# Kernel tuning notes

Hardware: AMD Instinct MI355X
Metric: run time of the kernel (lower is better)

The kernel has to match this reference:

```python
import jax, jax.numpy as jnp
import numpy as np

W_MSE = 0.5  # config['training']['mse']


def setup_inputs() -> dict:
    key = jax.random.key(0)
    k1, k2 = jax.random.split(key)
    num_q, num_p = 128, 1024
    pred = jax.random.normal(k1, (num_q, num_p), dtype=jnp.float32)
    y = jax.random.randint(k2, (num_q, num_p), 0, 2, dtype=jnp.int32)
    return {"pred": pred, "y": y}


def reference(pred, y):
    num_q, num_p = pred.shape
    yf = (y == 1).astype(pred.dtype)          # relevance mask [q, p]
    non_rel = 1.0 - yf
    # MarginRankingLoss(margin=0) with x1=pred[i,j] (relevant), x2=pred[i,:],
    # target=(y!=1): per-element contribution is relu(pred[i,p]-pred[i,j]) for
    # non-relevant p, 0 for relevant p; mean over p, summed over relevant j.
    # D[i,p,j] = relu(pred[i,p] - pred[i,j])
    D = jnp.maximum(pred[:, :, None] - pred[:, None, :], 0.0)  # [q, p, j]
    loss_per_q = jnp.einsum('qpj,qp,qj->q', D, non_rel, yf) / num_p  # [q]
    rank_term = loss_per_q.mean()
    # BCEWithLogitsLoss(pred, y), numerically stable
    bce = jnp.mean(jnp.maximum(pred, 0.0) - pred * yf
                   + jnp.log1p(jnp.exp(-jnp.abs(pred))))
    return -(1.0 - W_MSE) * rank_term + W_MSE * bce
```

## Files before the change

### kernel.cpp

```cpp
#include <hip/hip_runtime.h>
#include <math.h>


constexpr int NQ = 128;
constexpr int NP = 1024;
constexpr int BLK = 1024;

__global__ __launch_bounds__(BLK)
void mmrl_main_kernel(const float* __restrict__ pred,
                      const int* __restrict__ y,
                      float* __restrict__ ws) {
    __shared__ float sp[NP];
    __shared__ float syf[NP];
    __shared__ float red_r[BLK / 64];
    __shared__ float red_b[BLK / 64];

    const int q = blockIdx.x;
    const int tid = threadIdx.x;

    sp[tid] = pred[q * NP + tid];
    syf[tid] = (y[q * NP + tid] == 1) ? 1.0f : 0.0f;
    __syncthreads();

    const float x = sp[tid];
    const float yf = syf[tid];

    float bce = fmaxf(x, 0.0f) - x * yf + log1pf(expf(-fabsf(x)));

    float rank = 0.0f;
    #pragma unroll 8
    for (int j = 0; j < NP; ++j) {
        rank += fmaxf(x - sp[j], 0.0f) * syf[j];
    }
    rank *= (1.0f - yf);

    #pragma unroll
    for (int off = 32; off > 0; off >>= 1) {
        rank += __shfl_down(rank, off, 64);
        bce  += __shfl_down(bce,  off, 64);
    }
    const int wave = tid >> 6;
    const int lane = tid & 63;
    if (lane == 0) { red_r[wave] = rank; red_b[wave] = bce; }
    __syncthreads();

    if (tid == 0) {
        float r = 0.0f, b = 0.0f;
        #pragma unroll
        for (int w = 0; w < BLK / 64; ++w) { r += red_r[w]; b += red_b[w]; }
        atomicAdd(&ws[0], r);
        atomicAdd(&ws[1], b);
    }
}

__global__ void mmrl_finalize_kernel(const float* __restrict__ ws,
                                     float* __restrict__ out) {
    const float scale = 1.0f / (float)(NQ * NP);
    const float rank_term = ws[0] * scale;
    const float bce = ws[1] * scale;
    out[0] = -0.5f * rank_term + 0.5f * bce;
}

extern "C" void kernel_launch(void* const* d_in, const int* in_sizes, int n_in,
                              void* d_out, int out_size, void* d_ws, size_t ws_size,
                              hipStream_t stream) {
    const float* pred = (const float*)d_in[0];
    const int*   y    = (const int*)d_in[1];
    float* ws  = (float*)d_ws;
    float* out = (float*)d_out;

    hipMemsetAsync(ws, 0, 2 * sizeof(float), stream);

    mmrl_main_kernel<<<NQ, BLK, 0, stream>>>(pred, y, ws);
    mmrl_finalize_kernel<<<1, 1, 0, stream>>>(ws, out);
}
```

Baseline: 78.03 us.

## Compact relevant scores per query, split rows across blocks, broadcast via readlane

Each block now gathers only the relevant pred values of its query into a compacted shared list, padded with large sentinels, so the inner pairwise loop runs over about half as many j. Work is split into 4 blocks of 256 threads per query, giving 512 blocks instead of 128. The inner loop broadcasts values with readlane from registers instead of reading shared memory, and uses four accumulators. The memset and atomics are replaced by per-block partials and a tree-reduction finalize kernel. The cost is that each of the 4 blocks per query redundantly builds the full compacted list, and summation order now depends on the order of shared atomics.

```diff
diff --git a/kernel.cpp b/kernel.cpp
--- a/kernel.cpp
+++ b/kernel.cpp
@@ -2,37 +2,68 @@
 #include <math.h>
 
 
-constexpr int NQ = 128;
-constexpr int NP = 1024;
-constexpr int BLK = 1024;
+constexpr int NQ  = 128;
+constexpr int NP  = 1024;
+constexpr int BLK = 256;
+constexpr int SPLIT = NP / BLK;
+constexpr int GRID = NQ * SPLIT;
 
 __global__ __launch_bounds__(BLK)
 void mmrl_main_kernel(const float* __restrict__ pred,
                       const int* __restrict__ y,
-                      float* __restrict__ ws) {
-    __shared__ float sp[NP];
-    __shared__ float syf[NP];
+                      float* __restrict__ partial_r,
+                      float* __restrict__ partial_b) {
+    __shared__ float sj_list[NP + 64];
+    __shared__ int   s_cnt;
     __shared__ float red_r[BLK / 64];
     __shared__ float red_b[BLK / 64];
 
-    const int q = blockIdx.x;
+    const int bid = blockIdx.x;
+    const int q   = bid >> 2;
+    const int sub = bid & (SPLIT - 1);
     const int tid = threadIdx.x;
+    const int lane = tid & 63;
 
-    sp[tid] = pred[q * NP + tid];
-    syf[tid] = (y[q * NP + tid] == 1) ? 1.0f : 0.0f;
+    if (tid == 0) s_cnt = 0;
     __syncthreads();
 
-    const float x = sp[tid];
-    const float yf = syf[tid];
+    const float4 p4 = *reinterpret_cast<const float4*>(pred + q * NP + tid * 4);
+    const int4   y4 = *reinterpret_cast<const int4*>(y + q * NP + tid * 4);
+    float vals[4];
+    int c = 0;
+    if (y4.x == 1) vals[c++] = p4.x;
+    if (y4.y == 1) vals[c++] = p4.y;
+    if (y4.z == 1) vals[c++] = p4.z;
+    if (y4.w == 1) vals[c++] = p4.w;
+    int base = 0;
+    if (c > 0) base = atomicAdd(&s_cnt, c);
+    for (int k = 0; k < c; ++k) sj_list[base + k] = vals[k];
+    __syncthreads();
+
+    const int n    = s_cnt;
+    const int npad = (n + 63) & ~63;
+    if (tid < npad - n) sj_list[n + tid] = 1e30f;
+    __syncthreads();
+
+    const int   pidx = sub * BLK + tid;
+    const float x    = pred[q * NP + pidx];
+    const int   yv   = y[q * NP + pidx];
+    const float yf   = (yv == 1) ? 1.0f : 0.0f;
 
     float bce = fmaxf(x, 0.0f) - x * yf + log1pf(expf(-fabsf(x)));
 
-    float rank = 0.0f;
-    #pragma unroll 8
-    for (int j = 0; j < NP; ++j) {
-        rank += fmaxf(x - sp[j], 0.0f) * syf[j];
+    float r0 = 0.0f, r1 = 0.0f, r2 = 0.0f, r3 = 0.0f;
+    for (int jc = 0; jc < npad; jc += 64) {
+        const int sji = __float_as_int(sj_list[jc + lane]);
+        #pragma unroll
+        for (int l = 0; l < 64; l += 4) {
+            r0 += fmaxf(x - __int_as_float(__builtin_amdgcn_readlane(sji, l + 0)), 0.0f);
+            r1 += fmaxf(x - __int_as_float(__builtin_amdgcn_readlane(sji, l + 1)), 0.0f);
+            r2 += fmaxf(x - __int_as_float(__builtin_amdgcn_readlane(sji, l + 2)), 0.0f);
+            r3 += fmaxf(x - __int_as_float(__builtin_amdgcn_readlane(sji, l + 3)), 0.0f);
+        }
     }
-    rank *= (1.0f - yf);
+    float rank = ((r0 + r1) + (r2 + r3)) * (1.0f - yf);
 
     #pragma unroll
     for (int off = 32; off > 0; off >>= 1) {
@@ -40,25 +71,42 @@
         bce  += __shfl_down(bce,  off, 64);
     }
     const int wave = tid >> 6;
-    const int lane = tid & 63;
     if (lane == 0) { red_r[wave] = rank; red_b[wave] = bce; }
     __syncthreads();
-
     if (tid == 0) {
         float r = 0.0f, b = 0.0f;
         #pragma unroll
         for (int w = 0; w < BLK / 64; ++w) { r += red_r[w]; b += red_b[w]; }
-        atomicAdd(&ws[0], r);
-        atomicAdd(&ws[1], b);
+        partial_r[bid] = r;
+        partial_b[bid] = b;
     }
 }
 
-__global__ void mmrl_finalize_kernel(const float* __restrict__ ws,
-                                     float* __restrict__ out) {
-    const float scale = 1.0f / (float)(NQ * NP);
-    const float rank_term = ws[0] * scale;
-    const float bce = ws[1] * scale;
-    out[0] = -0.5f * rank_term + 0.5f * bce;
+__global__ __launch_bounds__(GRID)
+void mmrl_finalize_kernel(const float* __restrict__ partial_r,
+                          const float* __restrict__ partial_b,
+                          float* __restrict__ out) {
+    __shared__ float red_r[GRID / 64];
+    __shared__ float red_b[GRID / 64];
+    const int tid = threadIdx.x;
+    float r = partial_r[tid];
+    float b = partial_b[tid];
+    #pragma unroll
+    for (int off = 32; off > 0; off >>= 1) {
+        r += __shfl_down(r, off, 64);
+        b += __shfl_down(b, off, 64);
+    }
+    const int wave = tid >> 6;
+    const int lane = tid & 63;
+    if (lane == 0) { red_r[wave] = r; red_b[wave] = b; }
+    __syncthreads();
+    if (tid == 0) {
+        float rs = 0.0f, bs = 0.0f;
+        #pragma unroll
+        for (int w = 0; w < GRID / 64; ++w) { rs += red_r[w]; bs += red_b[w]; }
+        const float scale = 1.0f / (float)(NQ * NP);
+        out[0] = -0.5f * (rs * scale) + 0.5f * (bs * scale);
+    }
 }
 
 extern "C" void kernel_launch(void* const* d_in, const int* in_sizes, int n_in,
@@ -66,11 +114,10 @@
                               hipStream_t stream) {
     const float* pred = (const float*)d_in[0];
     const int*   y    = (const int*)d_in[1];
-    float* ws  = (float*)d_ws;
+    float* partial_r = (float*)d_ws;
+    float* partial_b = partial_r + GRID;
     float* out = (float*)d_out;
 
-    hipMemsetAsync(ws, 0, 2 * sizeof(float), stream);
-
-    mmrl_main_kernel<<<NQ, BLK, 0, stream>>>(pred, y, ws);
-    mmrl_finalize_kernel<<<1, 1, 0, stream>>>(ws, out);
+    mmrl_main_kernel<<<GRID, BLK, 0, stream>>>(pred, y, partial_r, partial_b);
+    mmrl_finalize_kernel<<<1, GRID, 0, stream>>>(partial_r, partial_b, out);
 }
```

Result: faster. 66.82 us (-14.4%).
